# Optimization experiments

Hardware: AMD Instinct MI355X
Metric: run time of the kernel (lower is better)

## Reference

```python
import jax, jax.numpy as jnp
import numpy as np

PAD = 1
NMS_DIST = 4
BORDER_DIST = 4
TOP_K = 500
DET_THRESH = 0.8


def _conv(x, w, b, pad):
    y = jax.lax.conv_general_dilated(
        x, w, window_strides=(1, 1), padding=[(pad, pad), (pad, pad)],
        dimension_numbers=("NCHW", "OIHW", "NCHW"))
    return y + b[None, :, None, None]


def setup_inputs() -> dict:
    key = jax.random.key(0)
    ks = jax.random.split(key, 10)
    B, C, H, W = 2, 1, 384, 384

    def w(k, o, i, s):
        return jax.random.normal(k, (o, i, s, s), jnp.float32) * (1.0 / np.sqrt(i * s * s))

    return {
        "images": jax.random.uniform(ks[0], (B, C, H, W), jnp.float32),
        "bb_w1": w(ks[1], 64, 1, 3), "bb_b1": jnp.zeros((64,), jnp.float32),
        "bb_w2": w(ks[2], 64, 64, 3), "bb_b2": jnp.zeros((64,), jnp.float32),
        "bb_w3": w(ks[3], 128, 64, 3), "bb_b3": jnp.zeros((128,), jnp.float32),
        "bb_w4": w(ks[4], 128, 128, 3), "bb_b4": jnp.zeros((128,), jnp.float32),
        "det_w1": w(ks[5], 128, 128, 3), "det_b1": jnp.zeros((128,), jnp.float32),
        "det_w2": w(ks[6], 1, 128, 1), "det_b2": jnp.zeros((1,), jnp.float32),
        "des_w1": w(ks[7], 256, 128, 3), "des_b1": jnp.zeros((256,), jnp.float32),
        "des_w2": w(ks[8], 128, 256, 1), "des_b2": jnp.zeros((128,), jnp.float32),
        "scale_factor": jnp.float32(1.0),
    }


def reference(images, bb_w1, bb_b1, bb_w2, bb_b2, bb_w3, bb_b3, bb_w4, bb_b4,
              det_w1, det_b1, det_w2, det_b2, des_w1, des_b1, des_w2, des_b2,
              scale_factor):
    relu = jax.nn.relu
    x = relu(_conv(images, bb_w1, bb_b1, PAD))
    x = relu(_conv(x, bb_w2, bb_b2, PAD))
    x = relu(_conv(x, bb_w3, bb_b3, PAD))
    feats = relu(_conv(x, bb_w4, bb_b4, PAD))  # [B,128,H,W]

    # Detector head: 3x3 conv+ReLU, then 1x1 conv -> logits [B,1,H,W]
    d = relu(_conv(feats, det_w1, det_b1, PAD))
    logits = _conv(d, det_w2, det_b2, 0)

    # Descriptor head: 3x3 conv+ReLU (lat=256), then 1x1 conv -> raw descriptors [B,D,H,W]
    e = relu(_conv(feats, des_w1, des_b1, PAD))
    raw = _conv(e, des_w2, des_b2, 0)

    # MagicPoint post-processing (cell_size=1): prob = sigmoid(logits)
    prob = jax.nn.sigmoid(logits[:, 0])  # [B,H,W]
    B, H, W = prob.shape

    # Box NMS via max-pool: keep local maxima above threshold, suppress borders
    win = 2 * NMS_DIST + 1
    pooled = jax.lax.reduce_window(prob, -jnp.inf, jax.lax.max,
                                   (1, win, win), (1, 1, 1), "SAME")
    ys = jnp.arange(H)
    xs = jnp.arange(W)
    border = ((ys >= BORDER_DIST) & (ys < H - BORDER_DIST))[:, None] \
           & ((xs >= BORDER_DIST) & (xs < W - BORDER_DIST))[None, :]
    nms_prob = jnp.where((prob >= pooled) & (prob > DET_THRESH) & border, prob, 0.0)

    # Fixed top-k keypoints per image
    flat = nms_prob.reshape(B, H * W)
    topv, topi = jax.lax.top_k(flat, TOP_K)  # [B,K]
    y = (topi // W).astype(jnp.float32)
    xp = (topi % W).astype(jnp.float32)
    positions = jnp.stack([y, xp, topv], axis=-1)  # [B,K,3] (row, col, prob)

    # sparsify_descriptors: gather raw descriptors at keypoint locations, L2-normalize
    D = raw.shape[1]
    raw_flat = raw.reshape(B, D, H * W)
    desc = jnp.take_along_axis(raw_flat, topi[:, None, :], axis=2)  # [B,D,K]
    desc = jnp.swapaxes(desc, 1, 2)  # [B,K,D]
    norm = jnp.maximum(jnp.linalg.norm(desc, axis=-1, keepdims=True), 1e-12)
    sparse_descriptors = scale_factor * desc / norm
    return sparse_descriptors, positions
```

## Files before the change

### kernel.cpp

```cpp
#include <hip/hip_runtime.h>
#include <hip/hip_bf16.h>

#define DEVI __device__ __forceinline__

typedef __bf16 bf16x8 __attribute__((ext_vector_type(8)));
typedef float  f32x4  __attribute__((ext_vector_type(4)));
typedef unsigned short ushort_t;

static constexpr int H = 384, W = 384, BATCH = 2, HW = H * W;
static constexpr int NMSD = 4, BORD = 4, TOPK = 500;
static constexpr float THRESH = 0.8f;
static constexpr int CAP = 2048;
static constexpr int SORTN = 2048;

DEVI ushort_t f2b(float f) {
  __hip_bfloat16 h = __float2bfloat16(f);
  ushort_t s;
  __builtin_memcpy(&s, &h, 2);
  return s;
}
DEVI float b2f(ushort_t u) { return __uint_as_float(((unsigned)u) << 16); }

DEVI void gload_lds16(const void* g, void* l) {
  __builtin_amdgcn_global_load_lds((const __attribute__((address_space(1))) void*)g,
                                   (__attribute__((address_space(3))) void*)l,
                                   16, 0, 0);
}

DEVI void wfrag_one(const float* __restrict__ src, ushort_t* __restrict__ dst,
                    int d, int COC, int CCC, int CIN) {
  int j = d & 7, l = (d >> 3) & 63, rest = d >> 9;
  int ccc = rest % CCC;
  int t2 = rest / CCC;
  int coc = t2 % COC, t = t2 / COC;
  int co = coc * 16 + (l & 15), ci = ccc * 32 + (l >> 4) * 8 + j;
  dst[d] = f2b(src[((size_t)co * CIN + ci) * 9 + t]);
}

__global__ __launch_bounds__(256) void setup_all(
    const float* __restrict__ w2s, ushort_t* __restrict__ wp2,
    const float* __restrict__ w3s, ushort_t* __restrict__ wp3,
    const float* __restrict__ w4s, ushort_t* __restrict__ wp4,
    const float* __restrict__ wds, ushort_t* __restrict__ wpd,
    const float* __restrict__ dw1, ushort_t* __restrict__ w1t,
    const float* __restrict__ dw2, float* __restrict__ w2t,
    ushort_t* __restrict__ zer, int* __restrict__ cnt) {
  int d = blockIdx.x * 256 + threadIdx.x;
  if (d < 1024) { zer[d] = 0; if (d < 2) cnt[d] = 0; return; }
  d -= 1024;
  if (d < 36864)  { wfrag_one(w2s, wp2, d, 4, 2, 64);  return; }
  d -= 36864;
  if (d < 73728)  { wfrag_one(w3s, wp3, d, 8, 2, 64);  return; }
  d -= 73728;
  if (d < 147456) { wfrag_one(w4s, wp4, d, 8, 4, 128); return; }
  d -= 147456;
  if (d < 147456) { wfrag_one(wds, wpd, d, 8, 4, 128); return; }
  d -= 147456;
  if (d < 294912) {
    int o = d / 1152, k = d % 1152;
    w1t[(size_t)(k >> 2) * 1024 + o * 4 + (k & 3)] = f2b(dw1[d]);
    return;
  }
  d -= 294912;
  if (d < 32768) {
    int o = d / 128, c = d % 128;
    w2t[d] = dw2[c * 256 + o];
  }
}

__global__ __launch_bounds__(256) void conv1_kernel(
    const float* __restrict__ img, const float* __restrict__ w,
    const float* __restrict__ bias, ushort_t* __restrict__ xout) {
  __shared__ __align__(16) float wt[9 * 64];
  __shared__ float bs[64];
  const int tid = threadIdx.x;
  for (int j = tid; j < 576; j += 256) {
    int co = j / 9, t = j % 9;
    wt[t * 64 + co] = w[j];
  }
  if (tid < 64) bs[tid] = bias[tid];
  __syncthreads();

  const int p = blockIdx.x * 256 + tid;
  const int b = p / HW, rem = p % HW;
  const int y = rem / W, x = rem % W;

  float in[9];
#pragma unroll
  for (int t = 0; t < 9; ++t) {
    int yy = y + t / 3 - 1, xx = x + t % 3 - 1;
    in[t] = (yy >= 0 && yy < H && xx >= 0 && xx < W) ? img[(size_t)b * HW + yy * W + xx] : 0.f;
  }
  float acc[64];
#pragma unroll
  for (int c = 0; c < 64; ++c) acc[c] = bs[c];
#pragma unroll
  for (int t = 0; t < 9; ++t) {
    float v = in[t];
#pragma unroll
    for (int c4 = 0; c4 < 16; ++c4) {
      float4 w4 = *reinterpret_cast<const float4*>(&wt[t * 64 + c4 * 4]);
      acc[c4 * 4 + 0] += w4.x * v;
      acc[c4 * 4 + 1] += w4.y * v;
      acc[c4 * 4 + 2] += w4.z * v;
      acc[c4 * 4 + 3] += w4.w * v;
    }
  }
  ushort_t* op = xout + (size_t)p * 64;
#pragma unroll
  for (int g = 0; g < 8; ++g) {
    uint4 u;
    u.x = (unsigned)f2b(fmaxf(acc[g * 8 + 0], 0.f)) | ((unsigned)f2b(fmaxf(acc[g * 8 + 1], 0.f)) << 16);
    u.y = (unsigned)f2b(fmaxf(acc[g * 8 + 2], 0.f)) | ((unsigned)f2b(fmaxf(acc[g * 8 + 3], 0.f)) << 16);
    u.z = (unsigned)f2b(fmaxf(acc[g * 8 + 4], 0.f)) | ((unsigned)f2b(fmaxf(acc[g * 8 + 5], 0.f)) << 16);
    u.w = (unsigned)f2b(fmaxf(acc[g * 8 + 6], 0.f)) | ((unsigned)f2b(fmaxf(acc[g * 8 + 7], 0.f)) << 16);
    *reinterpret_cast<uint4*>(op + g * 8) = u;
  }
}

template <int CIN, int COUT>
__global__ __launch_bounds__(256) void conv3x3_mfma(
    const ushort_t* __restrict__ xin, const ushort_t* __restrict__ wp,
    const float* __restrict__ bias, ushort_t* __restrict__ xout,
    const ushort_t* __restrict__ zer) {
  constexpr int NT = 192;
  constexpr int MFRAG = COUT / 16;
  constexpr int NFRAG = 3;
  constexpr int CC = CIN / 32;
  constexpr int COC = COUT / 16;
  constexpr int P = 3 * CC;
  constexpr int BCH = 13;

  __shared__ __align__(16) ushort_t lB[2][BCH * 512];

  const int x0 = (blockIdx.x % (W / NT)) * NT;
  const int y = blockIdx.x / (W / NT);
  const int b = blockIdx.y;

  const int tid = threadIdx.x;
  const int wid = tid >> 6, lane = tid & 63;
  const int wc = wid;
  const int l4 = lane >> 2;
  const int lb8 = (lane & 3) * 8;
  const int kg = lane >> 4;
  const int lr = lane & 15;

  const f32x4 fz = {0.f, 0.f, 0.f, 0.f};
  f32x4 acc[MFRAG][NFRAG];
#pragma unroll
  for (int m = 0; m < MFRAG; ++m)
#pragma unroll
    for (int n = 0; n < NFRAG; ++n) acc[m][n] = fz;

  auto stage = [&](int p) {
    const int dyi = p / CC, ccc = p % CC, pb = p & 1;
    const int yy = y + dyi - 1;
    const bool rowok = (yy >= 0) && (yy < H);
    const ushort_t* srow = xin + ((size_t)(b * H + yy) * W) * CIN + ccc * 32;
    for (int ch = wid; ch < BCH; ch += 4) {
      int row = ch * 16 + l4;
      int xx = x0 - 1 + row;
      const ushort_t* src = (rowok && row < 194 && xx >= 0 && xx < W)
                                ? srow + (size_t)xx * CIN + lb8
                                : zer + lb8;
      gload_lds16(src, &lB[pb][ch * 512]);
    }
  };

  stage(0);
#pragma unroll 1
  for (int p = 0; p < P; ++p) {
    __syncthreads();
    if (p + 1 < P) stage(p + 1);
    const int dyi = p / CC, ccc = p % CC, pb = p & 1;
    const ushort_t* wbase = wp + ((size_t)(dyi * 3) * COC * CC + ccc) * 512 + lane * 8;
    const ushort_t* lbb = &lB[pb][0];
#pragma unroll
    for (int tt = 0; tt < 3; ++tt) {
      bf16x8 af[MFRAG];
#pragma unroll
      for (int m = 0; m < MFRAG; ++m)
        af[m] = *reinterpret_cast<const bf16x8*>(
            wbase + ((size_t)tt * COC * CC + m * CC) * 512);
      bf16x8 bfr[NFRAG];
#pragma unroll
      for (int n = 0; n < NFRAG; ++n)
        bfr[n] = *reinterpret_cast<const bf16x8*>(
            &lbb[(wc * 48 + n * 16 + lr + tt) * 32 + kg * 8]);
#pragma unroll
      for (int m = 0; m < MFRAG; ++m)
#pragma unroll
        for (int n = 0; n < NFRAG; ++n)
          acc[m][n] = __builtin_amdgcn_mfma_f32_16x16x32_bf16(af[m], bfr[n], acc[m][n], 0, 0, 0);
    }
  }

  const int lq = lane >> 4;
  ushort_t* orow = xout + ((size_t)(b * H + y) * W) * COUT;
#pragma unroll
  for (int m = 0; m < MFRAG; ++m) {
    const int co = m * 16 + lq * 4;
    const float4 bv = *reinterpret_cast<const float4*>(&bias[co]);
#pragma unroll
    for (int n = 0; n < NFRAG; ++n) {
      const int px = x0 + wc * 48 + n * 16 + lr;
      f32x4 v = acc[m][n];
      ushort4 pk;
      pk.x = f2b(fmaxf(v[0] + bv.x, 0.f));
      pk.y = f2b(fmaxf(v[1] + bv.y, 0.f));
      pk.z = f2b(fmaxf(v[2] + bv.z, 0.f));
      pk.w = f2b(fmaxf(v[3] + bv.w, 0.f));
      *reinterpret_cast<ushort4*>(&orow[(size_t)px * COUT + co]) = pk;
    }
  }
}

__global__ __launch_bounds__(384) void det2_rowmax(
    const ushort_t* __restrict__ dbuf, const float* __restrict__ w2,
    const float* __restrict__ b2, float* __restrict__ prob,
    float* __restrict__ tmp) {
  __shared__ float ws[128];
  __shared__ float pr[W];
  const int tid = threadIdx.x;
  if (tid < 128) ws[tid] = w2[tid];
  __syncthreads();
  const int p = blockIdx.x * W + tid;
  const ushort_t* dp = dbuf + (size_t)p * 128;
  float acc = b2[0];
#pragma unroll
  for (int k = 0; k < 128; k += 8) {
    uint4 q = *reinterpret_cast<const uint4*>(dp + k);
    acc += __uint_as_float(q.x << 16) * ws[k + 0];
    acc += __uint_as_float(q.x & 0xffff0000u) * ws[k + 1];
    acc += __uint_as_float(q.y << 16) * ws[k + 2];
    acc += __uint_as_float(q.y & 0xffff0000u) * ws[k + 3];
    acc += __uint_as_float(q.z << 16) * ws[k + 4];
    acc += __uint_as_float(q.z & 0xffff0000u) * ws[k + 5];
    acc += __uint_as_float(q.w << 16) * ws[k + 6];
    acc += __uint_as_float(q.w & 0xffff0000u) * ws[k + 7];
  }
  float pv = 1.f / (1.f + expf(-acc));
  prob[p] = pv;
  pr[tid] = pv;
  __syncthreads();
  float m = -1e30f;
#pragma unroll
  for (int d = -NMSD; d <= NMSD; ++d) {
    int xx = tid + d;
    if (xx >= 0 && xx < W) m = fmaxf(m, pr[xx]);
  }
  tmp[p] = m;
}

__global__ __launch_bounds__(256) void colmax9_cand(
    const float* __restrict__ tmp, const float* __restrict__ prob,
    int* __restrict__ cnt, float* __restrict__ candv, int* __restrict__ candi) {
  const int p = blockIdx.x * 256 + threadIdx.x;
  const int b = p / HW, rem = p % HW;
  const int y = rem / W, x = rem % W;
  float m = -1e30f;
#pragma unroll
  for (int d = -NMSD; d <= NMSD; ++d) {
    int yy = y + d;
    if (yy >= 0 && yy < H) m = fmaxf(m, tmp[(size_t)b * HW + yy * W + x]);
  }
  float pv = prob[p];
  bool keep = (pv >= m) && (pv > THRESH) &&
              (y >= BORD) && (y < H - BORD) && (x >= BORD) && (x < W - BORD);
  if (keep) {
    int pos = atomicAdd(&cnt[b], 1);
    if (pos < CAP) {
      candv[b * CAP + pos] = pv;
      candi[b * CAP + pos] = rem;
    }
  }
}

__global__ __launch_bounds__(256) void select_topk(
    const int* __restrict__ cnt, const float* __restrict__ candv,
    const int* __restrict__ candi, float* __restrict__ pos_out,
    int* __restrict__ topi_g) {
  __shared__ float sv[SORTN];
  __shared__ int si[SORTN];
  __shared__ int tail[TOPK];
  const int b = blockIdx.x, tid = threadIdx.x;
  int nc = cnt[b];
  if (nc > CAP) nc = CAP;
  for (int j = tid; j < SORTN; j += 256) {
    if (j < nc) {
      sv[j] = candv[b * CAP + j];
      si[j] = candi[b * CAP + j];
    } else {
      sv[j] = -1.f;
      si[j] = 0x7fffffff;
    }
  }
  __syncthreads();
  if (nc > 0) {
    for (int k = 2; k <= SORTN; k <<= 1) {
      for (int j = k >> 1; j > 0; j >>= 1) {
        for (int i = tid; i < SORTN; i += 256) {
          int l = i ^ j;
          if (l > i) {
            float vi = sv[i], vl = sv[l];
            int ii = si[i], il = si[l];
            bool i_better = (vi > vl) || (vi == vl && ii < il);
            bool desc = ((i & k) == 0);
            bool sw = desc ? (!i_better) : i_better;
            if (sw) {
              sv[i] = vl; sv[l] = vi;
              si[i] = il; si[l] = ii;
            }
          }
        }
        __syncthreads();
      }
    }
  }
  if (tid == 0) {
    int need = TOPK - nc;
    if (need < 0) need = 0;
    int idx = 0, filled = 0;
    while (filled < need && idx < HW) {
      bool used = false;
      for (int q = 0; q < nc; ++q)
        if (si[q] == idx) { used = true; break; }
      if (!used) tail[filled++] = idx;
      ++idx;
    }
  }
  __syncthreads();
  for (int k2 = tid; k2 < TOPK; k2 += 256) {
    float v; int idx;
    if (k2 < nc) { v = sv[k2]; idx = si[k2]; }
    else         { v = 0.f;    idx = tail[k2 - nc]; }
    pos_out[((size_t)b * TOPK + k2) * 3 + 0] = (float)(idx / W);
    pos_out[((size_t)b * TOPK + k2) * 3 + 1] = (float)(idx % W);
    pos_out[((size_t)b * TOPK + k2) * 3 + 2] = v;
    topi_g[b * TOPK + k2] = idx;
  }
}

__global__ __launch_bounds__(256) void des_head(
    const ushort_t* __restrict__ feats, const int* __restrict__ topi_g,
    const ushort_t* __restrict__ w1t, const float* __restrict__ b1,
    const float* __restrict__ w2t, const float* __restrict__ b2,
    const float* __restrict__ scale, float* __restrict__ desc_out) {
  __shared__ __align__(16) float xf[1152];
  __shared__ __align__(16) float es[256];
  __shared__ float rs[128];
  __shared__ float nrm_s;
  const int g = blockIdx.x;
  const int b = g / TOPK;
  const int tid = threadIdx.x;
  const int idx = topi_g[g];
  const int y = idx / W, x = idx % W;
  for (int j = tid; j < 1152; j += 256) {
    int ci = j / 9, t = j % 9;
    int yy = y + t / 3 - 1, xx = x + t % 3 - 1;
    xf[j] = (yy >= 0 && yy < H && xx >= 0 && xx < W)
                ? b2f(feats[((size_t)(b * H + yy) * W + xx) * 128 + ci])
                : 0.f;
  }
  __syncthreads();
  float e = b1[tid];
  const ushort4* w4p = reinterpret_cast<const ushort4*>(w1t);
#pragma unroll 4
  for (int k4 = 0; k4 < 288; ++k4) {
    ushort4 wv = w4p[(size_t)k4 * 256 + tid];
    float4 x4 = *reinterpret_cast<const float4*>(&xf[k4 * 4]);
    e += b2f(wv.x) * x4.x + b2f(wv.y) * x4.y + b2f(wv.z) * x4.z + b2f(wv.w) * x4.w;
  }
  es[tid] = fmaxf(e, 0.f);
  __syncthreads();
  if (tid < 128) {
    float r = b2[tid];
#pragma unroll 4
    for (int o = 0; o < 256; ++o) r += es[o] * w2t[o * 128 + tid];
    rs[tid] = r;
  }
  __syncthreads();
  if (tid < 64) {
    float v = rs[tid] * rs[tid] + rs[tid + 64] * rs[tid + 64];
    for (int off = 32; off > 0; off >>= 1) v += __shfl_down(v, off);
    if (tid == 0) nrm_s = sqrtf(v);
  }
  __syncthreads();
  if (tid < 128) {
    float nrm = fmaxf(nrm_s, 1e-12f);
    desc_out[(size_t)g * 128 + tid] = rs[tid] * (scale[0] / nrm);
  }
}

extern "C" void kernel_launch(void* const* d_in, const int* in_sizes, int n_in,
                              void* d_out, int out_size, void* d_ws, size_t ws_size,
                              hipStream_t stream) {
  (void)in_sizes; (void)n_in; (void)out_size; (void)ws_size;
  const float* images = (const float*)d_in[0];
  const float* bbw1 = (const float*)d_in[1];  const float* bbb1 = (const float*)d_in[2];
  const float* bbw2 = (const float*)d_in[3];  const float* bbb2 = (const float*)d_in[4];
  const float* bbw3 = (const float*)d_in[5];  const float* bbb3 = (const float*)d_in[6];
  const float* bbw4 = (const float*)d_in[7];  const float* bbb4 = (const float*)d_in[8];
  const float* dtw1 = (const float*)d_in[9];  const float* dtb1 = (const float*)d_in[10];
  const float* dtw2 = (const float*)d_in[11]; const float* dtb2 = (const float*)d_in[12];
  const float* dsw1 = (const float*)d_in[13]; const float* dsb1 = (const float*)d_in[14];
  const float* dsw2 = (const float*)d_in[15]; const float* dsb2 = (const float*)d_in[16];
  const float* scale = (const float*)d_in[17];

  char* ws = (char*)d_ws;
  constexpr size_t SZ64 = (size_t)BATCH * HW * 64 * 2;
  constexpr size_t SZ128 = (size_t)BATCH * HW * 128 * 2;

  ushort_t* x1   = (ushort_t*)ws;
  ushort_t* x2   = (ushort_t*)(ws + SZ64);
  ushort_t* x3   = (ushort_t*)(ws + SZ128);
  ushort_t* fts  = (ushort_t*)ws;
  ushort_t* dbuf = (ushort_t*)(ws + SZ128);

  size_t off = 2 * SZ128;
  auto alloc = [&](size_t bytes) {
    char* p = ws + off;
    off = (off + bytes + 255) & ~(size_t)255;
    return p;
  };
  float* prob = (float*)alloc((size_t)BATCH * HW * 4);
  float* tmp  = (float*)alloc((size_t)BATCH * HW * 4);
  ushort_t* wp2 = (ushort_t*)alloc(9 * 64 * 64 * 2);
  ushort_t* wp3 = (ushort_t*)alloc(9 * 128 * 64 * 2);
  ushort_t* wp4 = (ushort_t*)alloc(9 * 128 * 128 * 2);
  ushort_t* wpd = (ushort_t*)alloc(9 * 128 * 128 * 2);
  ushort_t* w1t = (ushort_t*)alloc(288 * 256 * 4 * 2);
  float*    w2t = (float*)alloc(256 * 128 * 4);
  ushort_t* zer = (ushort_t*)alloc(2048);
  int* cnt      = (int*)alloc(256);
  float* candv  = (float*)alloc((size_t)BATCH * CAP * 4);
  int* candi    = (int*)alloc((size_t)BATCH * CAP * 4);
  int* topi_g   = (int*)alloc((size_t)BATCH * TOPK * 4);

  float* desc_out = (float*)d_out;
  float* pos_out  = (float*)d_out + (size_t)BATCH * TOPK * 128;

  setup_all<<<2868, 256, 0, stream>>>(bbw2, wp2, bbw3, wp3, bbw4, wp4, dtw1, wpd,
                                      dsw1, w1t, dsw2, w2t, zer, cnt);

  conv1_kernel<<<BATCH * HW / 256, 256, 0, stream>>>(images, bbw1, bbb1, x1);
  conv3x3_mfma<64, 64>  <<<dim3(2 * H, BATCH), 256, 0, stream>>>(x1, wp2, bbb2, x2, zer);
  conv3x3_mfma<64, 128> <<<dim3(2 * H, BATCH), 256, 0, stream>>>(x2, wp3, bbb3, x3, zer);
  conv3x3_mfma<128, 128><<<dim3(2 * H, BATCH), 256, 0, stream>>>(x3, wp4, bbb4, fts, zer);
  conv3x3_mfma<128, 128><<<dim3(2 * H, BATCH), 256, 0, stream>>>(fts, wpd, dtb1, dbuf, zer);

  det2_rowmax<<<BATCH * H, 384, 0, stream>>>(dbuf, dtw2, dtb2, prob, tmp);
  colmax9_cand<<<BATCH * HW / 256, 256, 0, stream>>>(tmp, prob, cnt, candv, candi);
  select_topk<<<BATCH, 256, 0, stream>>>(cnt, candv, candi, pos_out, topi_g);
  des_head<<<BATCH * TOPK, 256, 0, stream>>>(fts, topi_g, w1t, dsb1, w2t, dsb2, scale, desc_out);
}
```

Before: 567.6 us.

## Stage conv weights through LDS and tile warps over output channels and pixels

Result: faster. 547.5 us (-3.5%).

```diff
diff --git a/kernel.cpp b/kernel.cpp
--- a/kernel.cpp
+++ b/kernel.cpp
@@ -27,14 +27,12 @@
                                    16, 0, 0);
 }
 
-DEVI void wfrag_one(const float* __restrict__ src, ushort_t* __restrict__ dst,
-                    int d, int COC, int CCC, int CIN) {
-  int j = d & 7, l = (d >> 3) & 63, rest = d >> 9;
-  int ccc = rest % CCC;
-  int t2 = rest / CCC;
-  int coc = t2 % COC, t = t2 / COC;
-  int co = coc * 16 + (l & 15), ci = ccc * 32 + (l >> 4) * 8 + j;
-  dst[d] = f2b(src[((size_t)co * CIN + ci) * 9 + t]);
+DEVI void repack9(const float* __restrict__ src, ushort_t* __restrict__ dst,
+                  int d, int O, int I) {
+  int t = d / (O * I);
+  int r = d % (O * I);
+  int o = r / I, i = r % I;
+  dst[d] = f2b(src[(o * I + i) * 9 + t]);
 }
 
 __global__ __launch_bounds__(256) void setup_all(
@@ -48,13 +46,13 @@
   int d = blockIdx.x * 256 + threadIdx.x;
   if (d < 1024) { zer[d] = 0; if (d < 2) cnt[d] = 0; return; }
   d -= 1024;
-  if (d < 36864)  { wfrag_one(w2s, wp2, d, 4, 2, 64);  return; }
+  if (d < 36864)  { repack9(w2s, wp2, d, 64, 64);   return; }
   d -= 36864;
-  if (d < 73728)  { wfrag_one(w3s, wp3, d, 8, 2, 64);  return; }
+  if (d < 73728)  { repack9(w3s, wp3, d, 128, 64);  return; }
   d -= 73728;
-  if (d < 147456) { wfrag_one(w4s, wp4, d, 8, 4, 128); return; }
+  if (d < 147456) { repack9(w4s, wp4, d, 128, 128); return; }
   d -= 147456;
-  if (d < 147456) { wfrag_one(wds, wpd, d, 8, 4, 128); return; }
+  if (d < 147456) { repack9(wds, wpd, d, 128, 128); return; }
   d -= 147456;
   if (d < 294912) {
     int o = d / 1152, k = d % 1152;
@@ -118,20 +116,20 @@
   }
 }
 
-template <int CIN, int COUT>
+template <int CIN, int COUT, int MFRAG, int NFRAG>
 __global__ __launch_bounds__(256) void conv3x3_mfma(
     const ushort_t* __restrict__ xin, const ushort_t* __restrict__ wp,
     const float* __restrict__ bias, ushort_t* __restrict__ xout,
     const ushort_t* __restrict__ zer) {
-  constexpr int NT = 192;
-  constexpr int MFRAG = COUT / 16;
-  constexpr int NFRAG = 3;
+  constexpr int NT = 128;
+  constexpr int BROWS = 144;
   constexpr int CC = CIN / 32;
-  constexpr int COC = COUT / 16;
   constexpr int P = 3 * CC;
-  constexpr int BCH = 13;
-
-  __shared__ __align__(16) ushort_t lB[2][BCH * 512];
+  constexpr int ACH3 = 3 * COUT / 16;
+  constexpr int APW = ACH3 / 4;
+
+  __shared__ __align__(16) ushort_t lA[2][3 * COUT * 32];
+  __shared__ __align__(16) ushort_t lB[2][BROWS * 32];
 
   const int x0 = (blockIdx.x % (W / NT)) * NT;
   const int y = blockIdx.x / (W / NT);
@@ -139,7 +137,7 @@
 
   const int tid = threadIdx.x;
   const int wid = tid >> 6, lane = tid & 63;
-  const int wc = wid;
+  const int wr = wid >> 1, wc = wid & 1;
   const int l4 = lane >> 2;
   const int lb8 = (lane & 3) * 8;
   const int kg = lane >> 4;
@@ -157,10 +155,19 @@
     const int yy = y + dyi - 1;
     const bool rowok = (yy >= 0) && (yy < H);
     const ushort_t* srow = xin + ((size_t)(b * H + yy) * W) * CIN + ccc * 32;
-    for (int ch = wid; ch < BCH; ch += 4) {
+#pragma unroll
+    for (int j = 0; j < APW; ++j) {
+      int ch = wid * APW + j;
+      int row = ch * 16 + l4;
+      int tt = row / COUT, co = row % COUT;
+      const ushort_t* src =
+          wp + ((size_t)(dyi * 3 + tt) * COUT + co) * CIN + ccc * 32 + lb8;
+      gload_lds16(src, &lA[pb][ch * 512]);
+    }
+    for (int ch = wid; ch < 9; ch += 4) {
       int row = ch * 16 + l4;
       int xx = x0 - 1 + row;
-      const ushort_t* src = (rowok && row < 194 && xx >= 0 && xx < W)
+      const ushort_t* src = (rowok && row < 130 && xx >= 0 && xx < W)
                                 ? srow + (size_t)xx * CIN + lb8
                                 : zer + lb8;
       gload_lds16(src, &lB[pb][ch * 512]);
@@ -172,21 +179,18 @@
   for (int p = 0; p < P; ++p) {
     __syncthreads();
     if (p + 1 < P) stage(p + 1);
-    const int dyi = p / CC, ccc = p % CC, pb = p & 1;
-    const ushort_t* wbase = wp + ((size_t)(dyi * 3) * COC * CC + ccc) * 512 + lane * 8;
-    const ushort_t* lbb = &lB[pb][0];
+    const int pb = p & 1;
 #pragma unroll
     for (int tt = 0; tt < 3; ++tt) {
-      bf16x8 af[MFRAG];
+      bf16x8 af[MFRAG], bfr[NFRAG];
 #pragma unroll
       for (int m = 0; m < MFRAG; ++m)
         af[m] = *reinterpret_cast<const bf16x8*>(
-            wbase + ((size_t)tt * COC * CC + m * CC) * 512);
-      bf16x8 bfr[NFRAG];
+            &lA[pb][(tt * COUT + wr * MFRAG * 16 + m * 16 + lr) * 32 + kg * 8]);
 #pragma unroll
       for (int n = 0; n < NFRAG; ++n)
         bfr[n] = *reinterpret_cast<const bf16x8*>(
-            &lbb[(wc * 48 + n * 16 + lr + tt) * 32 + kg * 8]);
+            &lB[pb][(wc * NFRAG * 16 + n * 16 + lr + tt) * 32 + kg * 8]);
 #pragma unroll
       for (int m = 0; m < MFRAG; ++m)
 #pragma unroll
@@ -199,11 +203,11 @@
   ushort_t* orow = xout + ((size_t)(b * H + y) * W) * COUT;
 #pragma unroll
   for (int m = 0; m < MFRAG; ++m) {
-    const int co = m * 16 + lq * 4;
+    const int co = wr * MFRAG * 16 + m * 16 + lq * 4;
     const float4 bv = *reinterpret_cast<const float4*>(&bias[co]);
 #pragma unroll
     for (int n = 0; n < NFRAG; ++n) {
-      const int px = x0 + wc * 48 + n * 16 + lr;
+      const int px = x0 + wc * NFRAG * 16 + n * 16 + lr;
       f32x4 v = acc[m][n];
       ushort4 pk;
       pk.x = f2b(fmaxf(v[0] + bv.x, 0.f));
@@ -444,10 +448,10 @@
                                       dsw1, w1t, dsw2, w2t, zer, cnt);
 
   conv1_kernel<<<BATCH * HW / 256, 256, 0, stream>>>(images, bbw1, bbb1, x1);
-  conv3x3_mfma<64, 64>  <<<dim3(2 * H, BATCH), 256, 0, stream>>>(x1, wp2, bbb2, x2, zer);
-  conv3x3_mfma<64, 128> <<<dim3(2 * H, BATCH), 256, 0, stream>>>(x2, wp3, bbb3, x3, zer);
-  conv3x3_mfma<128, 128><<<dim3(2 * H, BATCH), 256, 0, stream>>>(x3, wp4, bbb4, fts, zer);
-  conv3x3_mfma<128, 128><<<dim3(2 * H, BATCH), 256, 0, stream>>>(fts, wpd, dtb1, dbuf, zer);
+  conv3x3_mfma<64, 64, 2, 4>  <<<dim3(3 * H, BATCH), 256, 0, stream>>>(x1, wp2, bbb2, x2, zer);
+  conv3x3_mfma<64, 128, 4, 4> <<<dim3(3 * H, BATCH), 256, 0, stream>>>(x2, wp3, bbb3, x3, zer);
+  conv3x3_mfma<128, 128, 4, 4><<<dim3(3 * H, BATCH), 256, 0, stream>>>(x3, wp4, bbb4, fts, zer);
+  conv3x3_mfma<128, 128, 4, 4><<<dim3(3 * H, BATCH), 256, 0, stream>>>(fts, wpd, dtb1, dbuf, zer);
 
   det2_rowmax<<<BATCH * H, 384, 0, stream>>>(dbuf, dtw2, dtb2, prob, tmp);
   colmax9_cand<<<BATCH * HW / 256, 256, 0, stream>>>(tmp, prob, cnt, candv, candi);
```
